# Performance work log

Measured on AMD Instinct MI355X. Metric: run time of the kernel, lower is better.

Reference implementation:

```python
import jax, jax.numpy as jnp
import numpy as np

N_NODES = 50000
N_EDGES = 800000
F_IN = 128
HID = 128
N_CLS = 10


def _gcn_conv(x, src, dst, n, W, b):
    # PyG GCNConv: h = x @ W, symmetric normalization with self-loops, scatter-add, + bias
    h = x @ W                                   # [N, H]
    deg = jax.ops.segment_sum(jnp.ones_like(dst, dtype=x.dtype), dst, num_segments=n)
    dinv = jnp.where(deg > 0, jax.lax.rsqrt(deg), 0.0)  # deg includes self-loops
    w = dinv[src] * dinv[dst]                   # [E+N]
    agg = jax.ops.segment_sum(h[src] * w[:, None], dst, num_segments=n)  # [N, H]
    return agg + b


def reference(x, edge_index, W1, b1, Ws1, bs1, W2, b2, Ws2, bs2, Wc, bc):
    n = x.shape[0]
    loops = jnp.arange(n, dtype=edge_index.dtype)
    src = jnp.concatenate([edge_index[0], loops])  # add self-loops
    dst = jnp.concatenate([edge_index[1], loops])

    x = jax.nn.relu(_gcn_conv(x, src, dst, n, W1, b1) + x @ Ws1 + bs1)
    x = jax.nn.relu(_gcn_conv(x, src, dst, n, W2, b2) + x @ Ws2 + bs2)

    x_avg = jnp.mean(x, axis=0, keepdims=True)  # [1, H]
    return x_avg @ Wc + bc                      # [1, C]


def setup_inputs() -> dict:
    key = jax.random.key(0)
    ks = jax.random.split(key, 12)
    s = 0.05
    return {
        "x": jax.random.normal(ks[0], (N_NODES, F_IN), jnp.float32),
        "edge_index": jax.random.randint(ks[1], (2, N_EDGES), 0, N_NODES, dtype=jnp.int64),
        "W1": jax.random.normal(ks[2], (F_IN, HID), jnp.float32) * s,
        "b1": jnp.zeros((HID,), jnp.float32),
        "Ws1": jax.random.normal(ks[3], (F_IN, HID), jnp.float32) * s,
        "bs1": jnp.zeros((HID,), jnp.float32),
        "W2": jax.random.normal(ks[4], (HID, HID), jnp.float32) * s,
        "b2": jnp.zeros((HID,), jnp.float32),
        "Ws2": jax.random.normal(ks[5], (HID, HID), jnp.float32) * s,
        "bs2": jnp.zeros((HID,), jnp.float32),
        "Wc": jax.random.normal(ks[6], (HID, N_CLS), jnp.float32) * s,
        "bc": jnp.zeros((N_CLS,), jnp.float32),
    }
```

## Files before the change

kernel.cpp:

```cpp
#include <hip/hip_runtime.h>

#define FEAT 128
#define N_CLS 10

typedef unsigned int uint;
typedef __attribute__((ext_vector_type(8))) short short8v;
typedef __attribute__((ext_vector_type(4))) float f32x4;

__device__ inline unsigned short f2bf(float f) {
    union { float f; uint u; } c; c.f = f;
    uint r = (c.u + 0x7FFFu + ((c.u >> 16) & 1u)) >> 16;
    return (unsigned short)r;
}
__device__ inline float bfhi(uint u) {
    union { uint u; float f; } c; c.u = u & 0xFFFF0000u;
    return c.f;
}
__device__ inline float bflo(uint u) {
    union { uint u; float f; } c; c.u = u << 16;
    return c.f;
}

__global__ void k_init(int* deg, float* colsum, int n) {
    int i = blockIdx.x * blockDim.x + threadIdx.x;
    if (i < n) deg[i] = 0;
    if (i < FEAT) colsum[i] = 0.f;
}

__global__ void k_hist(const int* __restrict__ dst, int* deg,
                       unsigned short* __restrict__ rank, int E) {
    int e = blockIdx.x * blockDim.x + threadIdx.x;
    if (e < E) {
        int r = atomicAdd(&deg[dst[e]], 1);
        rank[e] = (unsigned short)r;
    }
}

__global__ __launch_bounds__(256) void k_bsum(const int* __restrict__ deg,
                                              int* __restrict__ bsum, int n) {
    int i = blockIdx.x * 256 + threadIdx.x;
    int v = (i < n) ? deg[i] : 0;
    #pragma unroll
    for (int d = 32; d; d >>= 1) v += __shfl_down(v, d, 64);
    __shared__ int ws[4];
    int lane = threadIdx.x & 63, wid = threadIdx.x >> 6;
    if (lane == 0) ws[wid] = v;
    __syncthreads();
    if (threadIdx.x == 0) bsum[blockIdx.x] = ws[0] + ws[1] + ws[2] + ws[3];
}

__global__ __launch_bounds__(256) void k_bscan(int* bsum, int nb) {
    __shared__ int lds[256];
    int t = threadIdx.x;
    int v = (t < nb) ? bsum[t] : 0;
    lds[t] = v;
    __syncthreads();
    #pragma unroll
    for (int d = 1; d < 256; d <<= 1) {
        int u = (t >= d) ? lds[t - d] : 0;
        __syncthreads();
        lds[t] += u;
        __syncthreads();
    }
    if (t < nb) bsum[t] = lds[t] - v;
}

__global__ __launch_bounds__(256) void k_write(const int* __restrict__ deg,
                                               const int* __restrict__ bsum,
                                               int* off, float* dinv,
                                               int n, int E) {
    __shared__ int lds[256];
    int t = threadIdx.x;
    int i = blockIdx.x * 256 + t;
    int v = (i < n) ? deg[i] : 0;
    lds[t] = v;
    __syncthreads();
    #pragma unroll
    for (int d = 1; d < 256; d <<= 1) {
        int u = (t >= d) ? lds[t - d] : 0;
        __syncthreads();
        lds[t] += u;
        __syncthreads();
    }
    if (i < n) {
        off[i] = bsum[blockIdx.x] + (lds[t] - v);
        dinv[i] = rsqrtf((float)(deg[i] + 1));
    }
    if (i == n - 1) off[n] = E;
}

__global__ void k_fill(const int* __restrict__ src, const int* __restrict__ dst,
                       const unsigned short* __restrict__ rank,
                       const int* __restrict__ off, int* __restrict__ csr, int E) {
    int e = blockIdx.x * blockDim.x + threadIdx.x;
    if (e < E) {
        int d = dst[e];
        csr[off[d] + (int)rank[e]] = src[e];
    }
}

__global__ __launch_bounds__(256) void k_trans(const float* __restrict__ Wsrc,
                                               unsigned short* __restrict__ Wt) {
    int idx = blockIdx.x * 256 + threadIdx.x;
    int c = idx >> 7, k = idx & 127;
    Wt[c * FEAT + k] = f2bf(Wsrc[k * FEAT + c]);
}

__global__ __launch_bounds__(256) void k_gemm(
    const float* __restrict__ x, const unsigned short* __restrict__ Wt,
    const unsigned short* __restrict__ Wst, const float* __restrict__ b,
    const float* __restrict__ bs, const float* __restrict__ dinv,
    unsigned short* __restrict__ hs, float* __restrict__ xs, int n) {
    __shared__ unsigned short x_lds[64 * 136];
    int tid = threadIdx.x;
    int pair = blockIdx.x >> 1;
    int which = blockIdx.x & 1;
    int row0 = pair * 64;

    int c4 = (tid & 31) * 4;
    int rl = tid >> 5;
    #pragma unroll
    for (int p = 0; p < 8; ++p) {
        int r = rl + p * 8;
        float4 v = make_float4(0.f, 0.f, 0.f, 0.f);
        if (row0 + r < n) v = *(const float4*)&x[(size_t)(row0 + r) * FEAT + c4];
        uint2 pk;
        pk.x = (uint)f2bf(v.x) | ((uint)f2bf(v.y) << 16);
        pk.y = (uint)f2bf(v.z) | ((uint)f2bf(v.w) << 16);
        *(uint2*)&x_lds[r * 136 + c4] = pk;
    }

    int wv = tid >> 6;
    int lane = tid & 63;
    int lr = lane & 15;
    int lg = lane >> 4;
    int ctb = wv * 2;

    const unsigned short* Wp = which ? Wst : Wt;
    short8v wf[2][4];
    #pragma unroll
    for (int c = 0; c < 2; ++c)
        #pragma unroll
        for (int ks = 0; ks < 4; ++ks)
            wf[c][ks] = *(const short8v*)&Wp[(size_t)((ctb + c) * 16 + lr) * FEAT + ks * 32 + lg * 8];

    float4 bias[2];
    #pragma unroll
    for (int c = 0; c < 2; ++c) {
        int col = (ctb + c) * 16 + lg * 4;
        float4 bb  = *(const float4*)&b[col];
        float4 bb2 = *(const float4*)&bs[col];
        bias[c] = make_float4(bb.x + bb2.x, bb.y + bb2.y, bb.z + bb2.z, bb.w + bb2.w);
    }

    __syncthreads();

    #pragma unroll
    for (int ng = 0; ng < 4; ++ng) {
        short8v a[4];
        #pragma unroll
        for (int ks = 0; ks < 4; ++ks)
            a[ks] = *(const short8v*)&x_lds[(ng * 16 + lr) * 136 + ks * 32 + lg * 8];

        f32x4 acc[2];
        acc[0] = (f32x4){0.f, 0.f, 0.f, 0.f};
        acc[1] = (f32x4){0.f, 0.f, 0.f, 0.f};
        #pragma unroll
        for (int ks = 0; ks < 4; ++ks) {
            acc[0] = __builtin_amdgcn_mfma_f32_16x16x32_bf16(wf[0][ks], a[ks], acc[0], 0, 0, 0);
            acc[1] = __builtin_amdgcn_mfma_f32_16x16x32_bf16(wf[1][ks], a[ks], acc[1], 0, 0, 0);
        }

        int node = row0 + ng * 16 + lr;
        if (node < n) {
            if (which == 0) {
                float dv = dinv[node];
                #pragma unroll
                for (int c = 0; c < 2; ++c) {
                    int col = (ctb + c) * 16 + lg * 4;
                    uint2 pk;
                    pk.x = (uint)f2bf(acc[c][0] * dv) | ((uint)f2bf(acc[c][1] * dv) << 16);
                    pk.y = (uint)f2bf(acc[c][2] * dv) | ((uint)f2bf(acc[c][3] * dv) << 16);
                    *(uint2*)&hs[(size_t)node * FEAT + col] = pk;
                }
            } else {
                #pragma unroll
                for (int c = 0; c < 2; ++c) {
                    int col = (ctb + c) * 16 + lg * 4;
                    float4 o = make_float4(acc[c][0] + bias[c].x, acc[c][1] + bias[c].y,
                                           acc[c][2] + bias[c].z, acc[c][3] + bias[c].w);
                    *(float4*)&xs[(size_t)node * FEAT + col] = o;
                }
            }
        }
    }
}

__global__ __launch_bounds__(256) void k_agg(
    const unsigned short* __restrict__ hs, float* __restrict__ xs,
    const float* __restrict__ dinv, const int* __restrict__ off,
    const int* __restrict__ csr, int n) {
    int node = (blockIdx.x * 256 + threadIdx.x) >> 5;
    int sub = threadIdx.x & 31;
    if (node >= n) return;
    size_t fo = (size_t)sub * 4;
    const uint2* hp = (const uint2*)&hs[(size_t)node * FEAT + fo];
    uint2 p = *hp;
    float4 a0 = make_float4(bflo(p.x), bfhi(p.x), bflo(p.y), bfhi(p.y));
    float4 a1 = make_float4(0.f, 0.f, 0.f, 0.f);
    float4 a2 = make_float4(0.f, 0.f, 0.f, 0.f);
    float4 a3 = make_float4(0.f, 0.f, 0.f, 0.f);
    int s = off[node], e = off[node + 1];
    int j = s;
    for (; j + 4 <= e; j += 4) {
        int u0 = csr[j], u1 = csr[j + 1], u2 = csr[j + 2], u3 = csr[j + 3];
        uint2 q0 = *(const uint2*)&hs[(size_t)u0 * FEAT + fo];
        uint2 q1 = *(const uint2*)&hs[(size_t)u1 * FEAT + fo];
        uint2 q2 = *(const uint2*)&hs[(size_t)u2 * FEAT + fo];
        uint2 q3 = *(const uint2*)&hs[(size_t)u3 * FEAT + fo];
        a0.x += bflo(q0.x); a0.y += bfhi(q0.x); a0.z += bflo(q0.y); a0.w += bfhi(q0.y);
        a1.x += bflo(q1.x); a1.y += bfhi(q1.x); a1.z += bflo(q1.y); a1.w += bfhi(q1.y);
        a2.x += bflo(q2.x); a2.y += bfhi(q2.x); a2.z += bflo(q2.y); a2.w += bfhi(q2.y);
        a3.x += bflo(q3.x); a3.y += bfhi(q3.x); a3.z += bflo(q3.y); a3.w += bfhi(q3.y);
    }
    for (; j < e; ++j) {
        int u = csr[j];
        uint2 q = *(const uint2*)&hs[(size_t)u * FEAT + fo];
        a0.x += bflo(q.x); a0.y += bfhi(q.x); a0.z += bflo(q.y); a0.w += bfhi(q.y);
    }
    float4 acc;
    acc.x = (a0.x + a1.x) + (a2.x + a3.x);
    acc.y = (a0.y + a1.y) + (a2.y + a3.y);
    acc.z = (a0.z + a1.z) + (a2.z + a3.z);
    acc.w = (a0.w + a1.w) + (a2.w + a3.w);
    float dv = dinv[node];
    size_t o = (size_t)node * FEAT + fo;
    float4 sk = *(const float4*)&xs[o];
    float4 out;
    out.x = fmaxf(fmaf(acc.x, dv, sk.x), 0.f);
    out.y = fmaxf(fmaf(acc.y, dv, sk.y), 0.f);
    out.z = fmaxf(fmaf(acc.z, dv, sk.z), 0.f);
    out.w = fmaxf(fmaf(acc.w, dv, sk.w), 0.f);
    *(float4*)&xs[o] = out;
}

__global__ __launch_bounds__(256) void k_colsum(const float* __restrict__ x2,
                                                float* colsum, int n) {
    __shared__ float lds[256];
    int tid = threadIdx.x;
    int f = tid & 127;
    int half = tid >> 7;
    float acc = 0.f;
    for (int r = blockIdx.x * 2 + half; r < n; r += gridDim.x * 2)
        acc += x2[(size_t)r * FEAT + f];
    lds[tid] = acc;
    __syncthreads();
    if (tid < 128) atomicAdd(&colsum[f], lds[f] + lds[f + 128]);
}

__global__ void k_final(const float* __restrict__ colsum, const float* __restrict__ Wc,
                        const float* __restrict__ bc, float* out, int n) {
    int c = threadIdx.x;
    if (c < N_CLS) {
        float acc = 0.f;
        for (int f = 0; f < FEAT; ++f) acc += colsum[f] * Wc[f * N_CLS + c];
        out[c] = acc / (float)n + bc[c];
    }
}

extern "C" void kernel_launch(void* const* d_in, const int* in_sizes, int n_in,
                              void* d_out, int out_size, void* d_ws, size_t ws_size,
                              hipStream_t stream) {
    const float* x   = (const float*)d_in[0];
    const int*   ei  = (const int*)d_in[1];
    const float* W1  = (const float*)d_in[2];
    const float* b1  = (const float*)d_in[3];
    const float* Ws1 = (const float*)d_in[4];
    const float* bs1 = (const float*)d_in[5];
    const float* W2  = (const float*)d_in[6];
    const float* b2  = (const float*)d_in[7];
    const float* Ws2 = (const float*)d_in[8];
    const float* bs2 = (const float*)d_in[9];
    const float* Wc  = (const float*)d_in[10];
    const float* bc  = (const float*)d_in[11];
    float* out = (float*)d_out;

    const int n = in_sizes[0] / FEAT;
    const int E = in_sizes[1] / 2;
    const int* src = ei;
    const int* dst = ei + E;

    const int nb = (n + 255) / 256;

    char* w = (char*)d_ws;
    auto alloc = [&](size_t bytes) -> void* {
        void* p = (void*)w;
        w += (bytes + 255) & ~(size_t)255;
        return p;
    };
    int*   deg    = (int*)alloc((size_t)n * 4);
    int*   off    = (int*)alloc(((size_t)n + 1) * 4);
    int*   csr    = (int*)alloc((size_t)E * 4);
    unsigned short* rank = (unsigned short*)alloc((size_t)E * 2);
    float* dinv   = (float*)alloc((size_t)n * 4);
    float* colsum = (float*)alloc(FEAT * 4);
    int*   bsum   = (int*)alloc((size_t)nb * 4);
    unsigned short* Wt1  = (unsigned short*)alloc(FEAT * FEAT * 2);
    unsigned short* Wst1 = (unsigned short*)alloc(FEAT * FEAT * 2);
    unsigned short* Wt2  = (unsigned short*)alloc(FEAT * FEAT * 2);
    unsigned short* Wst2 = (unsigned short*)alloc(FEAT * FEAT * 2);
    unsigned short* A = (unsigned short*)alloc((size_t)n * FEAT * 2);
    float* B = (float*)alloc((size_t)n * FEAT * 4);
    float* C = (float*)alloc((size_t)n * FEAT * 4);

    k_init<<<nb, 256, 0, stream>>>(deg, colsum, n);
    k_hist<<<(E + 255) / 256, 256, 0, stream>>>(dst, deg, rank, E);
    k_bsum<<<nb, 256, 0, stream>>>(deg, bsum, n);
    k_bscan<<<1, 256, 0, stream>>>(bsum, nb);
    k_write<<<nb, 256, 0, stream>>>(deg, bsum, off, dinv, n, E);
    k_fill<<<(E + 255) / 256, 256, 0, stream>>>(src, dst, rank, off, csr, E);

    k_trans<<<64, 256, 0, stream>>>(W1, Wt1);
    k_trans<<<64, 256, 0, stream>>>(Ws1, Wst1);
    k_trans<<<64, 256, 0, stream>>>(W2, Wt2);
    k_trans<<<64, 256, 0, stream>>>(Ws2, Wst2);

    int gemm_grid = 2 * ((n + 63) / 64);
    int agg_grid  = (n + 7) / 8;

    k_gemm<<<gemm_grid, 256, 0, stream>>>(x, Wt1, Wst1, b1, bs1, dinv, A, B, n);
    k_agg<<<agg_grid, 256, 0, stream>>>(A, B, dinv, off, csr, n);
    k_gemm<<<gemm_grid, 256, 0, stream>>>(B, Wt2, Wst2, b2, bs2, dinv, A, C, n);
    k_agg<<<agg_grid, 256, 0, stream>>>(A, C, dinv, off, csr, n);

    k_colsum<<<512, 256, 0, stream>>>(C, colsum, n);
    k_final<<<1, 64, 0, stream>>>(colsum, Wc, bc, out, n);
}
```

Measured before the change: 296.7 us.

## Emit bf16 layer-1 output and fuse column-sum reduction into second aggregation

The first aggregation now writes its ReLU output as bf16 into a new buffer, and the second GEMM reads that bf16 input directly instead of reading fp32 and converting. The second aggregation reduces its outputs per block into partial column sums, so the full fp32 layer-2 activation is never written or re-read by the colsum kernel. The four weight-transpose launches are merged into one. This cuts global memory traffic and launch count. In exchange, the layer-1 activation is rounded to bf16 one step earlier, and colsum now reduces about 6250 partial rows.

```diff
diff --git a/kernel.cpp b/kernel.cpp
--- a/kernel.cpp
+++ b/kernel.cpp
@@ -4,13 +4,14 @@
 #define N_CLS 10
 
 typedef unsigned int uint;
+typedef unsigned short ushort;
 typedef __attribute__((ext_vector_type(8))) short short8v;
 typedef __attribute__((ext_vector_type(4))) float f32x4;
 
-__device__ inline unsigned short f2bf(float f) {
+__device__ inline ushort f2bf(float f) {
     union { float f; uint u; } c; c.f = f;
     uint r = (c.u + 0x7FFFu + ((c.u >> 16) & 1u)) >> 16;
-    return (unsigned short)r;
+    return (ushort)r;
 }
 __device__ inline float bfhi(uint u) {
     union { uint u; float f; } c; c.u = u & 0xFFFF0000u;
@@ -28,11 +29,11 @@
 }
 
 __global__ void k_hist(const int* __restrict__ dst, int* deg,
-                       unsigned short* __restrict__ rank, int E) {
+                       ushort* __restrict__ rank, int E) {
     int e = blockIdx.x * blockDim.x + threadIdx.x;
     if (e < E) {
         int r = atomicAdd(&deg[dst[e]], 1);
-        rank[e] = (unsigned short)r;
+        rank[e] = (ushort)r;
     }
 }
 
@@ -90,7 +91,7 @@
 }
 
 __global__ void k_fill(const int* __restrict__ src, const int* __restrict__ dst,
-                       const unsigned short* __restrict__ rank,
+                       const ushort* __restrict__ rank,
                        const int* __restrict__ off, int* __restrict__ csr, int E) {
     int e = blockIdx.x * blockDim.x + threadIdx.x;
     if (e < E) {
@@ -99,19 +100,26 @@
     }
 }
 
-__global__ __launch_bounds__(256) void k_trans(const float* __restrict__ Wsrc,
-                                               unsigned short* __restrict__ Wt) {
-    int idx = blockIdx.x * 256 + threadIdx.x;
+__global__ __launch_bounds__(256) void k_trans4(
+    const float* __restrict__ s0, const float* __restrict__ s1,
+    const float* __restrict__ s2, const float* __restrict__ s3,
+    ushort* __restrict__ d0, ushort* __restrict__ d1,
+    ushort* __restrict__ d2, ushort* __restrict__ d3) {
+    int m = blockIdx.x >> 6;
+    int idx = (blockIdx.x & 63) * 256 + threadIdx.x;
     int c = idx >> 7, k = idx & 127;
-    Wt[c * FEAT + k] = f2bf(Wsrc[k * FEAT + c]);
-}
-
+    const float* s = (m == 0) ? s0 : (m == 1) ? s1 : (m == 2) ? s2 : s3;
+    ushort* d = (m == 0) ? d0 : (m == 1) ? d1 : (m == 2) ? d2 : d3;
+    d[c * FEAT + k] = f2bf(s[k * FEAT + c]);
+}
+
+template <int BF16IN>
 __global__ __launch_bounds__(256) void k_gemm(
-    const float* __restrict__ x, const unsigned short* __restrict__ Wt,
-    const unsigned short* __restrict__ Wst, const float* __restrict__ b,
+    const void* __restrict__ xin, const ushort* __restrict__ Wt,
+    const ushort* __restrict__ Wst, const float* __restrict__ b,
     const float* __restrict__ bs, const float* __restrict__ dinv,
-    unsigned short* __restrict__ hs, float* __restrict__ xs, int n) {
-    __shared__ unsigned short x_lds[64 * 136];
+    ushort* __restrict__ hs, float* __restrict__ xs, int n) {
+    __shared__ ushort x_lds[64 * 136];
     int tid = threadIdx.x;
     int pair = blockIdx.x >> 1;
     int which = blockIdx.x & 1;
@@ -122,11 +130,16 @@
     #pragma unroll
     for (int p = 0; p < 8; ++p) {
         int r = rl + p * 8;
-        float4 v = make_float4(0.f, 0.f, 0.f, 0.f);
-        if (row0 + r < n) v = *(const float4*)&x[(size_t)(row0 + r) * FEAT + c4];
-        uint2 pk;
-        pk.x = (uint)f2bf(v.x) | ((uint)f2bf(v.y) << 16);
-        pk.y = (uint)f2bf(v.z) | ((uint)f2bf(v.w) << 16);
+        uint2 pk = make_uint2(0u, 0u);
+        if (row0 + r < n) {
+            if (BF16IN) {
+                pk = *(const uint2*)&((const ushort*)xin)[(size_t)(row0 + r) * FEAT + c4];
+            } else {
+                float4 v = *(const float4*)&((const float*)xin)[(size_t)(row0 + r) * FEAT + c4];
+                pk.x = (uint)f2bf(v.x) | ((uint)f2bf(v.y) << 16);
+                pk.y = (uint)f2bf(v.z) | ((uint)f2bf(v.w) << 16);
+            }
+        }
         *(uint2*)&x_lds[r * 136 + c4] = pk;
     }
 
@@ -136,7 +149,7 @@
     int lg = lane >> 4;
     int ctb = wv * 2;
 
-    const unsigned short* Wp = which ? Wst : Wt;
+    const ushort* Wp = which ? Wst : Wt;
     short8v wf[2][4];
     #pragma unroll
     for (int c = 0; c < 2; ++c)
@@ -196,52 +209,74 @@
     }
 }
 
+template <int MODE>
 __global__ __launch_bounds__(256) void k_agg(
-    const unsigned short* __restrict__ hs, float* __restrict__ xs,
+    const ushort* __restrict__ hs, const float* __restrict__ xs,
+    ushort* __restrict__ outb, float* __restrict__ psum,
     const float* __restrict__ dinv, const int* __restrict__ off,
     const int* __restrict__ csr, int n) {
-    int node = (blockIdx.x * 256 + threadIdx.x) >> 5;
-    int sub = threadIdx.x & 31;
-    if (node >= n) return;
+    int tid = threadIdx.x;
+    int node = (blockIdx.x * 256 + tid) >> 5;
+    int sub = tid & 31;
+    bool alive = node < n;
+    float4 out = make_float4(0.f, 0.f, 0.f, 0.f);
     size_t fo = (size_t)sub * 4;
-    const uint2* hp = (const uint2*)&hs[(size_t)node * FEAT + fo];
-    uint2 p = *hp;
-    float4 a0 = make_float4(bflo(p.x), bfhi(p.x), bflo(p.y), bfhi(p.y));
-    float4 a1 = make_float4(0.f, 0.f, 0.f, 0.f);
-    float4 a2 = make_float4(0.f, 0.f, 0.f, 0.f);
-    float4 a3 = make_float4(0.f, 0.f, 0.f, 0.f);
-    int s = off[node], e = off[node + 1];
-    int j = s;
-    for (; j + 4 <= e; j += 4) {
-        int u0 = csr[j], u1 = csr[j + 1], u2 = csr[j + 2], u3 = csr[j + 3];
-        uint2 q0 = *(const uint2*)&hs[(size_t)u0 * FEAT + fo];
-        uint2 q1 = *(const uint2*)&hs[(size_t)u1 * FEAT + fo];
-        uint2 q2 = *(const uint2*)&hs[(size_t)u2 * FEAT + fo];
-        uint2 q3 = *(const uint2*)&hs[(size_t)u3 * FEAT + fo];
-        a0.x += bflo(q0.x); a0.y += bfhi(q0.x); a0.z += bflo(q0.y); a0.w += bfhi(q0.y);
-        a1.x += bflo(q1.x); a1.y += bfhi(q1.x); a1.z += bflo(q1.y); a1.w += bfhi(q1.y);
-        a2.x += bflo(q2.x); a2.y += bfhi(q2.x); a2.z += bflo(q2.y); a2.w += bfhi(q2.y);
-        a3.x += bflo(q3.x); a3.y += bfhi(q3.x); a3.z += bflo(q3.y); a3.w += bfhi(q3.y);
-    }
-    for (; j < e; ++j) {
-        int u = csr[j];
-        uint2 q = *(const uint2*)&hs[(size_t)u * FEAT + fo];
-        a0.x += bflo(q.x); a0.y += bfhi(q.x); a0.z += bflo(q.y); a0.w += bfhi(q.y);
-    }
-    float4 acc;
-    acc.x = (a0.x + a1.x) + (a2.x + a3.x);
-    acc.y = (a0.y + a1.y) + (a2.y + a3.y);
-    acc.z = (a0.z + a1.z) + (a2.z + a3.z);
-    acc.w = (a0.w + a1.w) + (a2.w + a3.w);
-    float dv = dinv[node];
-    size_t o = (size_t)node * FEAT + fo;
-    float4 sk = *(const float4*)&xs[o];
-    float4 out;
-    out.x = fmaxf(fmaf(acc.x, dv, sk.x), 0.f);
-    out.y = fmaxf(fmaf(acc.y, dv, sk.y), 0.f);
-    out.z = fmaxf(fmaf(acc.z, dv, sk.z), 0.f);
-    out.w = fmaxf(fmaf(acc.w, dv, sk.w), 0.f);
-    *(float4*)&xs[o] = out;
+    if (alive) {
+        const uint2* hp = (const uint2*)&hs[(size_t)node * FEAT + fo];
+        uint2 p = *hp;
+        float4 a0 = make_float4(bflo(p.x), bfhi(p.x), bflo(p.y), bfhi(p.y));
+        float4 a1 = make_float4(0.f, 0.f, 0.f, 0.f);
+        float4 a2 = make_float4(0.f, 0.f, 0.f, 0.f);
+        float4 a3 = make_float4(0.f, 0.f, 0.f, 0.f);
+        int s = off[node], e = off[node + 1];
+        int j = s;
+        for (; j + 4 <= e; j += 4) {
+            int u0 = csr[j], u1 = csr[j + 1], u2 = csr[j + 2], u3 = csr[j + 3];
+            uint2 q0 = *(const uint2*)&hs[(size_t)u0 * FEAT + fo];
+            uint2 q1 = *(const uint2*)&hs[(size_t)u1 * FEAT + fo];
+            uint2 q2 = *(const uint2*)&hs[(size_t)u2 * FEAT + fo];
+            uint2 q3 = *(const uint2*)&hs[(size_t)u3 * FEAT + fo];
+            a0.x += bflo(q0.x); a0.y += bfhi(q0.x); a0.z += bflo(q0.y); a0.w += bfhi(q0.y);
+            a1.x += bflo(q1.x); a1.y += bfhi(q1.x); a1.z += bflo(q1.y); a1.w += bfhi(q1.y);
+            a2.x += bflo(q2.x); a2.y += bfhi(q2.x); a2.z += bflo(q2.y); a2.w += bfhi(q2.y);
+            a3.x += bflo(q3.x); a3.y += bfhi(q3.x); a3.z += bflo(q3.y); a3.w += bfhi(q3.y);
+        }
+        for (; j < e; ++j) {
+            int u = csr[j];
+            uint2 q = *(const uint2*)&hs[(size_t)u * FEAT + fo];
+            a0.x += bflo(q.x); a0.y += bfhi(q.x); a0.z += bflo(q.y); a0.w += bfhi(q.y);
+        }
+        float4 acc;
+        acc.x = (a0.x + a1.x) + (a2.x + a3.x);
+        acc.y = (a0.y + a1.y) + (a2.y + a3.y);
+        acc.z = (a0.z + a1.z) + (a2.z + a3.z);
+        acc.w = (a0.w + a1.w) + (a2.w + a3.w);
+        float dv = dinv[node];
+        float4 sk = *(const float4*)&xs[(size_t)node * FEAT + fo];
+        out.x = fmaxf(fmaf(acc.x, dv, sk.x), 0.f);
+        out.y = fmaxf(fmaf(acc.y, dv, sk.y), 0.f);
+        out.z = fmaxf(fmaf(acc.z, dv, sk.z), 0.f);
+        out.w = fmaxf(fmaf(acc.w, dv, sk.w), 0.f);
+    }
+    if (MODE == 0) {
+        if (alive) {
+            uint2 pk;
+            pk.x = (uint)f2bf(out.x) | ((uint)f2bf(out.y) << 16);
+            pk.y = (uint)f2bf(out.z) | ((uint)f2bf(out.w) << 16);
+            *(uint2*)&outb[(size_t)node * FEAT + fo] = pk;
+        }
+    } else {
+        __shared__ float sacc[8][FEAT];
+        int hw = tid >> 5;
+        *(float4*)&sacc[hw][sub * 4] = out;
+        __syncthreads();
+        if (tid < FEAT) {
+            float s = 0.f;
+            #pragma unroll
+            for (int h = 0; h < 8; ++h) s += sacc[h][tid];
+            psum[(size_t)blockIdx.x * FEAT + tid] = s;
+        }
+    }
 }
 
 __global__ __launch_bounds__(256) void k_colsum(const float* __restrict__ x2,
@@ -291,6 +326,7 @@
     const int* dst = ei + E;
 
     const int nb = (n + 255) / 256;
+    const int agg_grid = (n + 7) / 8;
 
     char* w = (char*)d_ws;
     auto alloc = [&](size_t bytes) -> void* {
@@ -301,17 +337,19 @@
     int*   deg    = (int*)alloc((size_t)n * 4);
     int*   off    = (int*)alloc(((size_t)n + 1) * 4);
     int*   csr    = (int*)alloc((size_t)E * 4);
-    unsigned short* rank = (unsigned short*)alloc((size_t)E * 2);
+    ushort* rank  = (ushort*)alloc((size_t)E * 2);
     float* dinv   = (float*)alloc((size_t)n * 4);
     float* colsum = (float*)alloc(FEAT * 4);
     int*   bsum   = (int*)alloc((size_t)nb * 4);
-    unsigned short* Wt1  = (unsigned short*)alloc(FEAT * FEAT * 2);
-    unsigned short* Wst1 = (unsigned short*)alloc(FEAT * FEAT * 2);
-    unsigned short* Wt2  = (unsigned short*)alloc(FEAT * FEAT * 2);
-    unsigned short* Wst2 = (unsigned short*)alloc(FEAT * FEAT * 2);
-    unsigned short* A = (unsigned short*)alloc((size_t)n * FEAT * 2);
-    float* B = (float*)alloc((size_t)n * FEAT * 4);
-    float* C = (float*)alloc((size_t)n * FEAT * 4);
+    float* psum   = (float*)alloc((size_t)agg_grid * FEAT * 4);
+    ushort* Wt1  = (ushort*)alloc(FEAT * FEAT * 2);
+    ushort* Wst1 = (ushort*)alloc(FEAT * FEAT * 2);
+    ushort* Wt2  = (ushort*)alloc(FEAT * FEAT * 2);
+    ushort* Wst2 = (ushort*)alloc(FEAT * FEAT * 2);
+    ushort* A = (ushort*)alloc((size_t)n * FEAT * 2);
+    float*  B = (float*)alloc((size_t)n * FEAT * 4);
+    float*  C = (float*)alloc((size_t)n * FEAT * 4);
+    ushort* D = (ushort*)alloc((size_t)n * FEAT * 2);
 
     k_init<<<nb, 256, 0, stream>>>(deg, colsum, n);
     k_hist<<<(E + 255) / 256, 256, 0, stream>>>(dst, deg, rank, E);
@@ -319,20 +357,15 @@
     k_bscan<<<1, 256, 0, stream>>>(bsum, nb);
     k_write<<<nb, 256, 0, stream>>>(deg, bsum, off, dinv, n, E);
     k_fill<<<(E + 255) / 256, 256, 0, stream>>>(src, dst, rank, off, csr, E);
-
-    k_trans<<<64, 256, 0, stream>>>(W1, Wt1);
-    k_trans<<<64, 256, 0, stream>>>(Ws1, Wst1);
-    k_trans<<<64, 256, 0, stream>>>(W2, Wt2);
-    k_trans<<<64, 256, 0, stream>>>(Ws2, Wst2);
+    k_trans4<<<256, 256, 0, stream>>>(W1, Ws1, W2, Ws2, Wt1, Wst1, Wt2, Wst2);
 
     int gemm_grid = 2 * ((n + 63) / 64);
-    int agg_grid  = (n + 7) / 8;
-
-    k_gemm<<<gemm_grid, 256, 0, stream>>>(x, Wt1, Wst1, b1, bs1, dinv, A, B, n);
-    k_agg<<<agg_grid, 256, 0, stream>>>(A, B, dinv, off, csr, n);
-    k_gemm<<<gemm_grid, 256, 0, stream>>>(B, Wt2, Wst2, b2, bs2, dinv, A, C, n);
-    k_agg<<<agg_grid, 256, 0, stream>>>(A, C, dinv, off, csr, n);
-
-    k_colsum<<<512, 256, 0, stream>>>(C, colsum, n);
+
+    k_gemm<0><<<gemm_grid, 256, 0, stream>>>(x, Wt1, Wst1, b1, bs1, dinv, A, B, n);
+    k_agg<0><<<agg_grid, 256, 0, stream>>>(A, B, D, nullptr, dinv, off, csr, n);
+    k_gemm<1><<<gemm_grid, 256, 0, stream>>>(D, Wt2, Wst2, b2, bs2, dinv, A, C, n);
+    k_agg<1><<<agg_grid, 256, 0, stream>>>(A, C, nullptr, psum, dinv, off, csr, n);
+
+    k_colsum<<<512, 256, 0, stream>>>(psum, colsum, agg_grid);
     k_final<<<1, 64, 0, stream>>>(colsum, Wc, bc, out, n);
 }
```

Result: faster. 284.5 us (-4.1%).
